# Kernel tuning notes

Hardware: AMD Instinct MI355X
Metric: run time of the kernel (lower is better)

The kernel has to match this reference:

```python
import jax, jax.numpy as jnp
import numpy as np

N_ATOMS = 100          # n_atoms from init_kwargs
BATCH = 1024           # dataset / batch size (single-batch usage per docstring)


def setup_inputs() -> dict:
    key = jax.random.key(0)
    k1, k2 = jax.random.split(key)
    # descriptors = pairwise distances between atoms -> 6 nonzero derivs per desc per frame
    ii, jj = np.triu_indices(N_ATOMS, 1)               # [D] each
    D = ii.shape[0]                                    # 4950 descriptors
    atoms = np.stack([ii, jj], axis=1)                 # [D, 2]
    atom_pd = np.repeat(atoms, 3, axis=1).reshape(-1)  # [D*6]: i,i,i,j,j,j per desc
    dim_pd = np.tile(np.array([0, 1, 2, 0, 1, 2]), D)  # [D*6]
    des_pd = np.repeat(np.arange(D), 6)                # [D*6]

    batch_ind = np.repeat(np.arange(BATCH), D * 6)     # [nnz]
    des_ind = np.tile(des_pd, BATCH)                   # [nnz]
    atom_ind = np.tile(atom_pd, BATCH)                 # [nnz]
    dim_ind = np.tile(dim_pd, BATCH)                   # [nnz]
    # faithful shifted index: per-frame offset + atom*3 + dim
    scatter_idx = batch_ind * (N_ATOMS * 3) + atom_ind * 3 + dim_ind

    nnz = batch_ind.shape[0]
    x = jax.random.normal(k1, (BATCH, D), dtype=jnp.float32)      # dq/d(descriptors)
    left = jax.random.normal(k2, (nnz,), dtype=jnp.float32)       # nonzero d(desc)/d(pos)
    return {
        "x": x,
        "left": left,
        "batch_ind": jnp.asarray(batch_ind, jnp.int32),
        "des_ind": jnp.asarray(des_ind, jnp.int32),
        "scatter_idx": jnp.asarray(scatter_idx, jnp.int32),
    }


def reference(x, left, batch_ind, des_ind, scatter_idx):
    # gather right operand: dq/d(desc) for each nonzero left entry
    right = x[batch_ind, des_ind]                      # [nnz]
    src = left * right                                 # chain rule terms
    # scatter-add into (frame, atom, dim) bins, then square (square modulus comps)
    acc = jax.ops.segment_sum(src, scatter_idx, num_segments=BATCH * N_ATOMS * 3)
    return (acc * acc).reshape(BATCH, N_ATOMS * 3)
```

## Files before the change

### kernel.cpp

```cpp
#include <hip/hip_runtime.h>
#include <math.h>


#define N_ATOMS 100
#define D_DESC  4950
#define NPAIR   (D_DESC / 2)
#define BATCH   1024
#define NOUT    (N_ATOMS * 3)

__device__ __forceinline__ int rowstart(int i) {
    return (i * (2 * N_ATOMS - 1 - i)) >> 1;
}

__global__ __launch_bounds__(512, 8)
void SmartDerivatives_kernel(const float* __restrict__ x,
                             const float* __restrict__ left,
                             float* __restrict__ out) {
    __shared__ float acc[NOUT];
    const int b   = blockIdx.x;
    const int tid = threadIdx.x;

    for (int t = tid; t < NOUT; t += 512) acc[t] = 0.0f;
    __syncthreads();

    const float* __restrict__ xb = x    + (size_t)b * D_DESC;
    const float* __restrict__ lb = left + (size_t)b * D_DESC * 6;

    const float4* __restrict__ lb4 = (const float4*)lb;
    const float2* __restrict__ xb2 = (const float2*)xb;
    for (int p = tid; p < NPAIR; p += 512) {
        const float4 q0 = lb4[(size_t)p * 3 + 0];
        const float4 q1 = lb4[(size_t)p * 3 + 1];
        const float4 q2 = lb4[(size_t)p * 3 + 2];
        const float2 xv = xb2[p];

        const int d0 = 2 * p;
        const float fr = 39601.0f - 8.0f * (float)d0;
        int i0 = (int)((199.0f - sqrtf(fr)) * 0.5f);
        while (rowstart(i0 + 1) <= d0) ++i0;
        while (rowstart(i0) > d0) --i0;
        const int j0 = d0 - rowstart(i0) + i0 + 1;
        const int j1 = (j0 < N_ATOMS - 1) ? (j0 + 1) : (i0 + 2);

        atomicAdd(&acc[j0 * 3 + 0], q0.w * xv.x);
        atomicAdd(&acc[j0 * 3 + 1], q1.x * xv.x);
        atomicAdd(&acc[j0 * 3 + 2], q1.y * xv.x);
        atomicAdd(&acc[j1 * 3 + 0], q2.y * xv.y);
        atomicAdd(&acc[j1 * 3 + 1], q2.z * xv.y);
        atomicAdd(&acc[j1 * 3 + 2], q2.w * xv.y);
    }

    const int wave = tid >> 6;
    const int lane = tid & 63;
    for (int a = wave; a < N_ATOMS - 1; a += 8) {
        const int rs  = rowstart(a);
        const int len = N_ATOMS - 1 - a;
        float s0 = 0.0f, s1 = 0.0f, s2 = 0.0f;
        for (int l = lane; l < len; l += 64) {
            const int d = rs + l;
            const float xv = xb[d];
            const float* lp = lb + (size_t)d * 6;
            s0 += lp[0] * xv;
            s1 += lp[1] * xv;
            s2 += lp[2] * xv;
        }
        #pragma unroll
        for (int off = 32; off > 0; off >>= 1) {
            s0 += __shfl_down(s0, off, 64);
            s1 += __shfl_down(s1, off, 64);
            s2 += __shfl_down(s2, off, 64);
        }
        if (lane == 0) {
            atomicAdd(&acc[a * 3 + 0], s0);
            atomicAdd(&acc[a * 3 + 1], s1);
            atomicAdd(&acc[a * 3 + 2], s2);
        }
    }

    __syncthreads();

    float* __restrict__ ob = out + (size_t)b * NOUT;
    for (int t = tid; t < NOUT; t += 512) {
        const float v = acc[t];
        ob[t] = v * v;
    }
}

extern "C" void kernel_launch(void* const* d_in, const int* in_sizes, int n_in,
                              void* d_out, int out_size, void* d_ws, size_t ws_size,
                              hipStream_t stream) {
    const float* x    = (const float*)d_in[0];
    const float* left = (const float*)d_in[1];
    float* out = (float*)d_out;
    SmartDerivatives_kernel<<<BATCH, 512, 0, stream>>>(x, left, out);
}
```

Before: 384.0 us.

## Split each frame across two blocks and combine partials in a second kernel

Each batch frame is now processed by two blocks, each covering half the descriptor pairs and alternating rows for the i-side reduction. Partial accumulators go to workspace, and a second kernel sums the two halves and squares them. Loads are also hoisted into registers up front (three pairs per thread) to raise memory-level parallelism, and the row loop is unrolled for up to two elements per lane. The aim is more blocks and more loads in flight to better saturate bandwidth, at the cost of an extra launch and a workspace round trip.

```diff
diff --git a/kernel.cpp b/kernel.cpp
--- a/kernel.cpp
+++ b/kernel.cpp
@@ -4,20 +4,22 @@
 
 #define N_ATOMS 100
 #define D_DESC  4950
-#define NPAIR   (D_DESC / 2)
+#define NPAIR   2475
 #define BATCH   1024
-#define NOUT    (N_ATOMS * 3)
+#define NOUT    300
+#define HALF0   1238
 
 __device__ __forceinline__ int rowstart(int i) {
     return (i * (2 * N_ATOMS - 1 - i)) >> 1;
 }
 
-__global__ __launch_bounds__(512, 8)
-void SmartDerivatives_kernel(const float* __restrict__ x,
-                             const float* __restrict__ left,
-                             float* __restrict__ out) {
+__global__ __launch_bounds__(512, 4)
+void sd_partial_kernel(const float* __restrict__ x,
+                       const float* __restrict__ left,
+                       float* __restrict__ ws) {
     __shared__ float acc[NOUT];
-    const int b   = blockIdx.x;
+    const int b   = blockIdx.x >> 1;
+    const int sub = blockIdx.x & 1;
     const int tid = threadIdx.x;
 
     for (int t = tid; t < NOUT; t += 512) acc[t] = 0.0f;
@@ -25,45 +27,66 @@
 
     const float* __restrict__ xb = x    + (size_t)b * D_DESC;
     const float* __restrict__ lb = left + (size_t)b * D_DESC * 6;
-
     const float4* __restrict__ lb4 = (const float4*)lb;
     const float2* __restrict__ xb2 = (const float2*)xb;
-    for (int p = tid; p < NPAIR; p += 512) {
-        const float4 q0 = lb4[(size_t)p * 3 + 0];
-        const float4 q1 = lb4[(size_t)p * 3 + 1];
-        const float4 q2 = lb4[(size_t)p * 3 + 2];
-        const float2 xv = xb2[p];
 
-        const int d0 = 2 * p;
-        const float fr = 39601.0f - 8.0f * (float)d0;
-        int i0 = (int)((199.0f - sqrtf(fr)) * 0.5f);
-        while (rowstart(i0 + 1) <= d0) ++i0;
-        while (rowstart(i0) > d0) --i0;
-        const int j0 = d0 - rowstart(i0) + i0 + 1;
-        const int j1 = (j0 < N_ATOMS - 1) ? (j0 + 1) : (i0 + 2);
-
-        atomicAdd(&acc[j0 * 3 + 0], q0.w * xv.x);
-        atomicAdd(&acc[j0 * 3 + 1], q1.x * xv.x);
-        atomicAdd(&acc[j0 * 3 + 2], q1.y * xv.x);
-        atomicAdd(&acc[j1 * 3 + 0], q2.y * xv.y);
-        atomicAdd(&acc[j1 * 3 + 1], q2.z * xv.y);
-        atomicAdd(&acc[j1 * 3 + 2], q2.w * xv.y);
+    const int pstart = sub * HALF0;
+    const int pend   = pstart + HALF0 - sub;
+    int    pk[3];
+    bool   vk[3];
+    float4 q0[3], q1[3], q2[3];
+    float2 xv[3];
+    #pragma unroll
+    for (int k = 0; k < 3; ++k) {
+        pk[k] = pstart + tid + 512 * k;
+        vk[k] = pk[k] < pend;
+        if (vk[k]) {
+            q0[k] = lb4[(size_t)pk[k] * 3 + 0];
+            q1[k] = lb4[(size_t)pk[k] * 3 + 1];
+            q2[k] = lb4[(size_t)pk[k] * 3 + 2];
+            xv[k] = xb2[pk[k]];
+        }
+    }
+    #pragma unroll
+    for (int k = 0; k < 3; ++k) {
+        if (vk[k]) {
+            const int d0 = 2 * pk[k];
+            const float fr = 39601.0f - 8.0f * (float)d0;
+            int i0 = (int)((199.0f - sqrtf(fr)) * 0.5f);
+            while (rowstart(i0 + 1) <= d0) ++i0;
+            while (rowstart(i0) > d0) --i0;
+            const int j0 = d0 - rowstart(i0) + i0 + 1;
+            const int j1 = (j0 < N_ATOMS - 1) ? (j0 + 1) : (i0 + 2);
+            atomicAdd(&acc[j0 * 3 + 0], q0[k].w * xv[k].x);
+            atomicAdd(&acc[j0 * 3 + 1], q1[k].x * xv[k].x);
+            atomicAdd(&acc[j0 * 3 + 2], q1[k].y * xv[k].x);
+            atomicAdd(&acc[j1 * 3 + 0], q2[k].y * xv[k].y);
+            atomicAdd(&acc[j1 * 3 + 1], q2[k].z * xv[k].y);
+            atomicAdd(&acc[j1 * 3 + 2], q2[k].w * xv[k].y);
+        }
     }
 
     const int wave = tid >> 6;
     const int lane = tid & 63;
-    for (int a = wave; a < N_ATOMS - 1; a += 8) {
+    for (int r = wave; ; r += 8) {
+        const int a = 2 * r + sub;
+        if (a >= N_ATOMS - 1) break;
         const int rs  = rowstart(a);
         const int len = N_ATOMS - 1 - a;
-        float s0 = 0.0f, s1 = 0.0f, s2 = 0.0f;
-        for (int l = lane; l < len; l += 64) {
-            const int d = rs + l;
-            const float xv = xb[d];
-            const float* lp = lb + (size_t)d * 6;
-            s0 += lp[0] * xv;
-            s1 += lp[1] * xv;
-            s2 += lp[2] * xv;
+        const int l0 = lane, l1 = lane + 64;
+        float a00 = 0, a01 = 0, a02 = 0, x0 = 0;
+        float a10 = 0, a11 = 0, a12 = 0, x1 = 0;
+        if (l0 < len) {
+            const float* lp = lb + (size_t)(rs + l0) * 6;
+            a00 = lp[0]; a01 = lp[1]; a02 = lp[2]; x0 = xb[rs + l0];
         }
+        if (l1 < len) {
+            const float* lp = lb + (size_t)(rs + l1) * 6;
+            a10 = lp[0]; a11 = lp[1]; a12 = lp[2]; x1 = xb[rs + l1];
+        }
+        float s0 = a00 * x0 + a10 * x1;
+        float s1 = a01 * x0 + a11 * x1;
+        float s2 = a02 * x0 + a12 * x1;
         #pragma unroll
         for (int off = 32; off > 0; off >>= 1) {
             s0 += __shfl_down(s0, off, 64);
@@ -79,11 +102,21 @@
 
     __syncthreads();
 
-    float* __restrict__ ob = out + (size_t)b * NOUT;
-    for (int t = tid; t < NOUT; t += 512) {
-        const float v = acc[t];
-        ob[t] = v * v;
-    }
+    float* __restrict__ wb = ws + ((size_t)sub * BATCH + b) * NOUT;
+    for (int t = tid; t < NOUT; t += 512) wb[t] = acc[t];
+}
+
+__global__ __launch_bounds__(256)
+void sd_combine_kernel(const float* __restrict__ ws, float* __restrict__ out) {
+    const int idx = blockIdx.x * 256 + threadIdx.x;
+    const float4 u = ((const float4*)ws)[idx];
+    const float4 v = ((const float4*)(ws + (size_t)BATCH * NOUT))[idx];
+    float4 o;
+    o.x = u.x + v.x; o.x *= o.x;
+    o.y = u.y + v.y; o.y *= o.y;
+    o.z = u.z + v.z; o.z *= o.z;
+    o.w = u.w + v.w; o.w *= o.w;
+    ((float4*)out)[idx] = o;
 }
 
 extern "C" void kernel_launch(void* const* d_in, const int* in_sizes, int n_in,
@@ -91,6 +124,9 @@
                               hipStream_t stream) {
     const float* x    = (const float*)d_in[0];
     const float* left = (const float*)d_in[1];
+    float* ws  = (float*)d_ws;
     float* out = (float*)d_out;
-    SmartDerivatives_kernel<<<BATCH, 512, 0, stream>>>(x, left, out);
+
+    sd_partial_kernel<<<BATCH * 2, 512, 0, stream>>>(x, left, ws);
+    sd_combine_kernel<<<(BATCH * NOUT / 4) / 256, 256, 0, stream>>>(ws, out);
 }
```

Result: slower. 393.2 us (+2.4%).
